# Optimization experiments

Hardware: AMD Instinct MI355X
Metric: run time of the kernel (lower is better)

Reference implementation:

```python
import jax, jax.numpy as jnp
import numpy as np

B, S, D = 256, 256, 1024
P = D // 2  # proj_dim default = input_dim / 2
NUM_HIDDEN = 2
EPS = 1e-7  # K.epsilon()
INIT_SCALE = 0.05  # keras 'uniform' init


def setup_inputs() -> dict:
    key = jax.random.key(0)
    ks = jax.random.split(key, 8)
    x = jax.random.normal(ks[0], (B, S, D), dtype=jnp.float32)
    mask = jax.random.randint(ks[1], (B, S), 0, 2).astype(bool)
    u = lambda k, shp: jax.random.uniform(k, shp, jnp.float32, -INIT_SCALE, INIT_SCALE)
    proj_head = u(ks[2], (D, P))
    proj_prep = u(ks[3], (D, P))
    proj_child = u(ks[4], (D, P))
    hidden_layers = u(ks[5], (NUM_HIDDEN, P, P))
    scorer = u(ks[6], (P,))
    return {"x": x, "proj_head": proj_head, "proj_prep": proj_prep,
            "proj_child": proj_child, "hidden_layers": hidden_layers,
            "scorer": scorer, "mask": mask}


def reference(x, proj_head, proj_prep, proj_child, hidden_layers, scorer, mask):
    # x: [B, S, D]; last two timesteps are preposition and child noun.
    head_enc = x[:, :-2, :]          # [B, S-2, D]
    prep_enc = x[:, -2, :]           # [B, D]
    child_enc = x[:, -1, :]          # [B, D]

    head_proj = jnp.einsum('bsd,dp->bsp', head_enc, proj_head)      # [B, S-2, P]
    prep_proj = (prep_enc @ proj_prep)[:, None, :]                  # [B, 1, P]
    child_proj = (child_enc @ proj_child)[:, None, :]               # [B, 1, P]

    # composition_type == 'HPCT'
    composed = jnp.tanh(head_proj + prep_proj + child_proj)         # [B, S-2, P]

    for i in range(hidden_layers.shape[0]):  # small fixed layer count
        composed = jnp.tanh(jnp.einsum('bsp,pq->bsq', composed, hidden_layers[i]))

    scores = jnp.einsum('bsp,p->bs', composed, scorer)              # [B, S-2]

    # masked exp-normalization (as in the original Keras code)
    exp_scores = jnp.exp(scores)
    head_mask = mask[:, :-2]
    masked_exp = jnp.where(head_mask, exp_scores, 0.0)
    exp_sum = jnp.sum(masked_exp, axis=1, keepdims=True) + EPS
    return masked_exp / exp_sum
```

## Files before the change

kernel.cpp:

```cpp
#include <hip/hip_runtime.h>
#include <hip/hip_bf16.h>
#include <stdint.h>

#define B_ 256
#define S_ 256
#define D_ 1024
#define P_ 512
#define SH 254
#define M_ (B_*SH)
#define EPSF 1e-7f

typedef __attribute__((ext_vector_type(8))) short short8v;
typedef __attribute__((ext_vector_type(4))) float float4v;

__device__ inline short f2bf(float f) {
  __hip_bfloat16 h = __float2bfloat16(f);
  return *reinterpret_cast<short*>(&h);
}
__device__ inline float fast_tanh(float x) {
  float e = __expf(2.0f * x);
  return 1.0f - 2.0f * __builtin_amdgcn_rcpf(e + 1.0f);
}

__global__ void k_detect(const unsigned char* m, int* flag) {
  __shared__ int c0, c3;
  if (threadIdx.x == 0) { c0 = 0; c3 = 0; }
  __syncthreads();
  int f0 = 0, f3 = 0;
  for (int i = threadIdx.x; i < 4096; i += 256) {
    unsigned char v = m[i];
    if (v != 0) {
      if ((i & 3) == 0) f0 = 1;
      if ((i & 3) == 3) f3 = 1;
    }
  }
  if (f0) atomicOr(&c0, 1);
  if (f3) atomicOr(&c3, 1);
  __syncthreads();
  if (threadIdx.x == 0) {
    int f;
    if (c3 == 0) f = 0;
    else if (c0 != 0) f = 1;
    else f = 2;
    *flag = f;
  }
}

__global__ void k_trans_head(const float* __restrict__ w, short* __restrict__ out) {
  int idx = blockIdx.x * 256 + threadIdx.x;
  int kc  = idx >> 13;
  int j   = idx & 8191;
  int krp = j >> 9;
  int n   = j & 511;
  int k0  = kc * 32 + krp * 2;
  unsigned lo = (unsigned short)f2bf(w[(size_t)k0 * P_ + n]);
  unsigned hi = (unsigned short)f2bf(w[(size_t)(k0 + 1) * P_ + n]);
  ((unsigned*)out)[kc * 8192 + n * 16 + krp] = lo | (hi << 16);
}

__global__ void k_trans_hidden(const float* __restrict__ h,
                               short* __restrict__ o0, short* __restrict__ o1) {
  int idx = blockIdx.x * 256 + threadIdx.x;
  int which = idx >> 17;
  int j = idx & 131071;
  int kc  = j >> 13;
  int r   = j & 8191;
  int krp = r >> 9;
  int n   = r & 511;
  const float* hs = h + (size_t)which * (P_*P_);
  int k0 = kc * 32 + krp * 2;
  unsigned lo = (unsigned short)f2bf(hs[(size_t)k0 * P_ + n]);
  unsigned hi = (unsigned short)f2bf(hs[(size_t)(k0 + 1) * P_ + n]);
  unsigned* o = (unsigned*)(which ? o1 : o0);
  o[kc * 8192 + n * 16 + krp] = lo | (hi << 16);
}

__global__ void __launch_bounds__(512) k_pc(const float* __restrict__ x,
                                            const float* __restrict__ wp,
                                            const float* __restrict__ wc,
                                            float* __restrict__ pc) {
  __shared__ float xs[16][256];
  int bg = blockIdx.x >> 4, cs = blockIdx.x & 15;
  int t = threadIdx.x;
  int bloc = t >> 5, c = t & 31;
  int batch = bg * 16 + bloc;
  int col = cs * 32 + c;
  float acc = 0.f;
  #pragma unroll
  for (int half = 0; half < 2; half++) {
    const float* wsrc = half ? wc : wp;
    for (int kc = 0; kc < 4; kc++) {
      const float* xr = x + ((size_t)(batch * S_ + SH + half)) * D_ + kc*256 + c*8;
      float4 v0 = *(const float4*)(xr + 0);
      float4 v1 = *(const float4*)(xr + 4);
      __syncthreads();
      *(float4*)&xs[bloc][c*8 + 0] = v0;
      *(float4*)&xs[bloc][c*8 + 4] = v1;
      __syncthreads();
      const float* wv = wsrc + (size_t)(kc*256) * P_ + col;
      #pragma unroll 8
      for (int d = 0; d < 256; d++) {
        acc += xs[bloc][d] * wv[(size_t)d * P_];
      }
    }
  }
  pc[batch * P_ + col] = acc;
}


#define LB2(DST, BASE, KC0) do {                                    \
  const uint4* _p = (BASE) + (size_t)(KC0)*2048 + bcol;             \
  DST[0]=_p[0];    DST[1]=_p[64];      DST[2]=_p[128];  DST[3]=_p[192]; \
  DST[4]=_p[2048]; DST[5]=_p[2048+64]; DST[6]=_p[2048+128]; DST[7]=_p[2048+192]; \
} while(0)

#define APAIR(CUR, CB, BUF) do {                                    \
  _Pragma("unroll") for (int cc = 0; cc < 2; cc++) {                \
    short8v a_[4];                                                  \
    _Pragma("unroll") for (int mt = 0; mt < 4; mt++)                \
      a_[mt] = *(const short8v*)&As[CUR][(mt*16 + l15)*136 + ((CB)+cc)*32 + quad*8]; \
    _Pragma("unroll") for (int nt = 0; nt < 4; nt++) {              \
      short8v bfr = *(short8v*)&BUF[cc*4 + nt];                     \
      _Pragma("unroll") for (int mt = 0; mt < 4; mt++)              \
        acc[mt][nt] = __builtin_amdgcn_mfma_f32_16x16x32_bf16(a_[mt], bfr, acc[mt][nt], 0, 0, 0); \
    }                                                               \
  }                                                                 \
} while(0)

#define S23(P, CURB, NXTB) do {                                     \
  if ((P) < 7) { LB2(NXTB, hb, 2*(P)+2); }                          \
  else if (stage == 0) { LB2(NXTB, h1v, 0); }                       \
  _Pragma("unroll") for (int cc = 0; cc < 2; cc++) {                \
    short8v a_[4];                                                  \
    _Pragma("unroll") for (int mt = 0; mt < 4; mt++)                \
      a_[mt] = *(const short8v*)&Cs[(mt*16 + l15)*520 + (2*(P)+cc)*32 + quad*8]; \
    _Pragma("unroll") for (int nt = 0; nt < 4; nt++) {              \
      short8v bfr = *(short8v*)&CURB[cc*4 + nt];                    \
      _Pragma("unroll") for (int mt = 0; mt < 4; mt++)              \
        acc[mt][nt] = __builtin_amdgcn_mfma_f32_16x16x32_bf16(a_[mt], bfr, acc[mt][nt], 0, 0, 0); \
    }                                                               \
  }                                                                 \
} while(0)

__global__ void __launch_bounds__(512, 2) k_main(
    const float* __restrict__ x, const short* __restrict__ wth,
    const short* __restrict__ h0t, const short* __restrict__ h1t,
    const float* __restrict__ scorer, const float* __restrict__ pc,
    float* __restrict__ scores)
{
  __shared__ __attribute__((aligned(16))) short As[2][64*136];
  __shared__ __attribute__((aligned(16))) short Cs[64*520];
  __shared__ float scorer_s[P_];
  __shared__ float pcs[2][P_];
  __shared__ float score_ws[64][8];

  const int tid  = threadIdx.x;
  const int lane = tid & 63;
  const int wn   = tid >> 6;
  const int l15  = lane & 15, quad = lane >> 4;
  const int rowbase = blockIdx.x * 64;

  scorer_s[tid] = scorer[tid];
  const int bb0 = rowbase / SH;
  const int bb1 = (rowbase + 63) / SH;
  pcs[0][tid] = pc[bb0 * P_ + tid];
  pcs[1][tid] = pc[bb1 * P_ + tid];
  const int lim1 = (bb0 + 1) * SH;

  const int arow = tid >> 3;
  const int akg  = (tid & 7) * 16;
  int r0 = rowbase + arow;
  int ab = r0 / SH;
  int as_ = r0 - ab * SH;
  const float* aptr = x + ((size_t)(ab * S_ + as_)) * D_ + akg;

  const uint4* wbv = (const uint4*)wth;
  const uint4* h0v = (const uint4*)h0t;
  const uint4* h1v = (const uint4*)h1t;
  const int bcol = (wn*64 + l15)*4 + quad;

  uint4 bA[8], bB[8];

  {
    float4 st0 = *(const float4*)(aptr + 0);
    float4 st1 = *(const float4*)(aptr + 4);
    float4 st2 = *(const float4*)(aptr + 8);
    float4 st3 = *(const float4*)(aptr + 12);
    short8v s0 = { f2bf(st0.x),f2bf(st0.y),f2bf(st0.z),f2bf(st0.w),
                   f2bf(st1.x),f2bf(st1.y),f2bf(st1.z),f2bf(st1.w) };
    short8v s1 = { f2bf(st2.x),f2bf(st2.y),f2bf(st2.z),f2bf(st2.w),
                   f2bf(st3.x),f2bf(st3.y),f2bf(st3.z),f2bf(st3.w) };
    *(short8v*)&As[0][arow*136 + akg]     = s0;
    *(short8v*)&As[0][arow*136 + akg + 8] = s1;
  }
  LB2(bA, wbv, 0);
  __syncthreads();

  float4v acc[4][4];
  #pragma unroll
  for (int i = 0; i < 4; i++)
    #pragma unroll
    for (int j = 0; j < 4; j++) acc[i][j] = (float4v){0.f,0.f,0.f,0.f};

  for (int sc = 0; sc < 8; sc++) {
    const int cur = sc & 1;
    float4 n0, n1, n2, n3;
    if (sc < 7) {
      const float* p = aptr + (sc + 1) * 128;
      n0 = *(const float4*)(p + 0);
      n1 = *(const float4*)(p + 4);
      n2 = *(const float4*)(p + 8);
      n3 = *(const float4*)(p + 12);
    }
    LB2(bB, wbv, 4*sc + 2);
    APAIR(cur, 0, bA);
    if (sc < 7) { LB2(bA, wbv, 4*sc + 4); }
    APAIR(cur, 2, bB);
    if (sc < 7) {
      short8v w0 = { f2bf(n0.x),f2bf(n0.y),f2bf(n0.z),f2bf(n0.w),
                     f2bf(n1.x),f2bf(n1.y),f2bf(n1.z),f2bf(n1.w) };
      short8v w1 = { f2bf(n2.x),f2bf(n2.y),f2bf(n2.z),f2bf(n2.w),
                     f2bf(n3.x),f2bf(n3.y),f2bf(n3.z),f2bf(n3.w) };
      *(short8v*)&As[cur ^ 1][arow*136 + akg]     = w0;
      *(short8v*)&As[cur ^ 1][arow*136 + akg + 8] = w1;
    }
    __syncthreads();
  }

  LB2(bA, h0v, 0);

  #pragma unroll
  for (int mt = 0; mt < 4; mt++) {
    #pragma unroll
    for (int j = 0; j < 4; j++) {
      int rl = mt*16 + quad*4 + j;
      int rg = rowbase + rl;
      const float* pcb = (rg >= lim1) ? pcs[1] : pcs[0];
      #pragma unroll
      for (int nt = 0; nt < 4; nt++) {
        int col = wn*64 + nt*16 + l15;
        float v = fast_tanh(acc[mt][nt][j] + pcb[col]);
        float o = __shfl_xor(v, 1, 64);
        unsigned hs = (unsigned short)f2bf(v);
        unsigned ho = (unsigned short)f2bf(o);
        if ((l15 & 1) == 0)
          *(unsigned*)&Cs[rl*520 + col] = hs | (ho << 16);
      }
    }
  }
  __syncthreads();

  #pragma unroll 1
  for (int stage = 0; stage < 2; stage++) {
    const uint4* hb = stage ? h1v : h0v;
    #pragma unroll
    for (int i = 0; i < 4; i++)
      #pragma unroll
      for (int j = 0; j < 4; j++) acc[i][j] = (float4v){0.f,0.f,0.f,0.f};

    S23(0, bA, bB); S23(1, bB, bA);
    S23(2, bA, bB); S23(3, bB, bA);
    S23(4, bA, bB); S23(5, bB, bA);
    S23(6, bA, bB); S23(7, bB, bA);

    if (stage == 0) {
      __syncthreads();
      #pragma unroll
      for (int mt = 0; mt < 4; mt++) {
        #pragma unroll
        for (int j = 0; j < 4; j++) {
          int rl = mt*16 + quad*4 + j;
          #pragma unroll
          for (int nt = 0; nt < 4; nt++) {
            int col = wn*64 + nt*16 + l15;
            float v = fast_tanh(acc[mt][nt][j]);
            float o = __shfl_xor(v, 1, 64);
            unsigned hs = (unsigned short)f2bf(v);
            unsigned ho = (unsigned short)f2bf(o);
            if ((l15 & 1) == 0)
              *(unsigned*)&Cs[rl*520 + col] = hs | (ho << 16);
          }
        }
      }
      __syncthreads();
    }
  }

  #pragma unroll
  for (int mt = 0; mt < 4; mt++) {
    #pragma unroll
    for (int j = 0; j < 4; j++) {
      float part = 0.f;
      #pragma unroll
      for (int nt = 0; nt < 4; nt++) {
        int col = wn*64 + nt*16 + l15;
        part += fast_tanh(acc[mt][nt][j]) * scorer_s[col];
      }
      #pragma unroll
      for (int o = 1; o < 16; o <<= 1) part += __shfl_xor(part, o, 64);
      if (l15 == 0) score_ws[mt*16 + quad*4 + j][wn] = part;
    }
  }
  __syncthreads();
  if (tid < 64) {
    float s = 0.f;
    #pragma unroll
    for (int k = 0; k < 8; k++) s += score_ws[tid][k];
    scores[rowbase + tid] = __expf(s);
  }
}

__global__ void __launch_bounds__(256) k_softmax(const float* __restrict__ scores,
                                                 const void* __restrict__ mask,
                                                 const int* __restrict__ flag,
                                                 float* __restrict__ out) {
  int b = blockIdx.x, t = threadIdx.x;
  int lane = t & 63, w = t >> 6;
  __shared__ float ps[4];
  float me = 0.f;
  bool valid = t < SH;
  if (valid) {
    float e = scores[b*SH + t];
    int f = *flag;
    bool mb;
    if (f == 1)      mb = ((const unsigned char*)mask)[b*S_ + t] != 0;
    else if (f == 2) mb = ((const float*)mask)[b*S_ + t] != 0.0f;
    else             mb = ((const int*)mask)[b*S_ + t] != 0;
    me = mb ? e : 0.f;
  }
  float v = me;
  for (int o = 1; o < 64; o <<= 1) v += __shfl_xor(v, o, 64);
  if (lane == 0) ps[w] = v;
  __syncthreads();
  float tot = ps[0] + ps[1] + ps[2] + ps[3] + EPSF;
  if (valid) out[b*SH + t] = me / tot;
}

extern "C" void kernel_launch(void* const* d_in, const int* in_sizes, int n_in,
                              void* d_out, int out_size, void* d_ws, size_t ws_size,
                              hipStream_t stream) {
  const float* x          = (const float*)d_in[0];
  const float* proj_head  = (const float*)d_in[1];
  const float* proj_prep  = (const float*)d_in[2];
  const float* proj_child = (const float*)d_in[3];
  const float* hidden     = (const float*)d_in[4];
  const float* scorer     = (const float*)d_in[5];
  const void*  mask       = d_in[6];
  float* out = (float*)d_out;
  char* ws = (char*)d_ws;

  int*   flag   = (int*)  (ws + 0);
  float* pc     = (float*)(ws + 256);
  short* wth    = (short*)(ws + 524544);
  short* h0t    = (short*)(ws + 1573120);
  short* h1t    = (short*)(ws + 2097408);
  float* scores = (float*)(ws + 2621696);

  k_detect<<<1, 256, 0, stream>>>((const unsigned char*)mask, flag);
  k_trans_head<<<1024, 256, 0, stream>>>(proj_head, wth);
  k_trans_hidden<<<1024, 256, 0, stream>>>(hidden, h0t, h1t);
  k_pc<<<256, 512, 0, stream>>>(x, proj_prep, proj_child, pc);
  k_main<<<1016, 512, 0, stream>>>(x, wth, h0t, h1t, scorer, pc, scores);
  k_softmax<<<256, 256, 0, stream>>>(scores, mask, flag, out);
}
```

Baseline: 695.3 us.

## Use 128-row tiles with 16 waves and load A directly from global

The main fused kernel now processes 128 rows per block with 1024 threads (16 waves, each owning 32 output columns) instead of 64 rows with 512 threads. The first GEMM drops the shared-memory double-buffered A staging: each wave loads its fp32 x fragments straight from global, converts them to bf16 in registers, and software-prefetches only the B fragments. The hidden-layer loops are simplified to one-step B prefetch loops. Every wave now reads the full 128xD A tile from global, so redundant global/L2 traffic rises 16x. Shared memory use also doubles, and register pressure under launch_bounds(1024,4) may limit occupancy or cause spills.

```diff
diff --git a/kernel.cpp b/kernel.cpp
--- a/kernel.cpp
+++ b/kernel.cpp
@@ -107,138 +107,85 @@
   pc[batch * P_ + col] = acc;
 }
 
-
-#define LB2(DST, BASE, KC0) do {                                    \
-  const uint4* _p = (BASE) + (size_t)(KC0)*2048 + bcol;             \
-  DST[0]=_p[0];    DST[1]=_p[64];      DST[2]=_p[128];  DST[3]=_p[192]; \
-  DST[4]=_p[2048]; DST[5]=_p[2048+64]; DST[6]=_p[2048+128]; DST[7]=_p[2048+192]; \
-} while(0)
-
-#define APAIR(CUR, CB, BUF) do {                                    \
-  _Pragma("unroll") for (int cc = 0; cc < 2; cc++) {                \
-    short8v a_[4];                                                  \
-    _Pragma("unroll") for (int mt = 0; mt < 4; mt++)                \
-      a_[mt] = *(const short8v*)&As[CUR][(mt*16 + l15)*136 + ((CB)+cc)*32 + quad*8]; \
-    _Pragma("unroll") for (int nt = 0; nt < 4; nt++) {              \
-      short8v bfr = *(short8v*)&BUF[cc*4 + nt];                     \
-      _Pragma("unroll") for (int mt = 0; mt < 4; mt++)              \
-        acc[mt][nt] = __builtin_amdgcn_mfma_f32_16x16x32_bf16(a_[mt], bfr, acc[mt][nt], 0, 0, 0); \
-    }                                                               \
-  }                                                                 \
-} while(0)
-
-#define S23(P, CURB, NXTB) do {                                     \
-  if ((P) < 7) { LB2(NXTB, hb, 2*(P)+2); }                          \
-  else if (stage == 0) { LB2(NXTB, h1v, 0); }                       \
-  _Pragma("unroll") for (int cc = 0; cc < 2; cc++) {                \
-    short8v a_[4];                                                  \
-    _Pragma("unroll") for (int mt = 0; mt < 4; mt++)                \
-      a_[mt] = *(const short8v*)&Cs[(mt*16 + l15)*520 + (2*(P)+cc)*32 + quad*8]; \
-    _Pragma("unroll") for (int nt = 0; nt < 4; nt++) {              \
-      short8v bfr = *(short8v*)&CURB[cc*4 + nt];                    \
-      _Pragma("unroll") for (int mt = 0; mt < 4; mt++)              \
-        acc[mt][nt] = __builtin_amdgcn_mfma_f32_16x16x32_bf16(a_[mt], bfr, acc[mt][nt], 0, 0, 0); \
-    }                                                               \
-  }                                                                 \
-} while(0)
-
-__global__ void __launch_bounds__(512, 2) k_main(
+__global__ void __launch_bounds__(1024, 4) k_main(
     const float* __restrict__ x, const short* __restrict__ wth,
     const short* __restrict__ h0t, const short* __restrict__ h1t,
     const float* __restrict__ scorer, const float* __restrict__ pc,
     float* __restrict__ scores)
 {
-  __shared__ __attribute__((aligned(16))) short As[2][64*136];
-  __shared__ __attribute__((aligned(16))) short Cs[64*520];
+  __shared__ __attribute__((aligned(16))) short Cs[128*520];
   __shared__ float scorer_s[P_];
   __shared__ float pcs[2][P_];
-  __shared__ float score_ws[64][8];
+  __shared__ float score_ws[128][16];
 
   const int tid  = threadIdx.x;
   const int lane = tid & 63;
-  const int wn   = tid >> 6;
+  const int w    = tid >> 6;
   const int l15  = lane & 15, quad = lane >> 4;
-  const int rowbase = blockIdx.x * 64;
-
-  scorer_s[tid] = scorer[tid];
+  const int rowbase = blockIdx.x * 128;
+
   const int bb0 = rowbase / SH;
-  const int bb1 = (rowbase + 63) / SH;
-  pcs[0][tid] = pc[bb0 * P_ + tid];
-  pcs[1][tid] = pc[bb1 * P_ + tid];
+  const int bb1 = (rowbase + 127) / SH;
+  if (tid < P_) {
+    scorer_s[tid] = scorer[tid];
+    pcs[0][tid] = pc[bb0 * P_ + tid];
+    pcs[1][tid] = pc[bb1 * P_ + tid];
+  }
   const int lim1 = (bb0 + 1) * SH;
 
-  const int arow = tid >> 3;
-  const int akg  = (tid & 7) * 16;
-  int r0 = rowbase + arow;
-  int ab = r0 / SH;
-  int as_ = r0 - ab * SH;
-  const float* aptr = x + ((size_t)(ab * S_ + as_)) * D_ + akg;
-
+  int aoff[8];
+  #pragma unroll
+  for (int mt = 0; mt < 8; mt++) {
+    int row = rowbase + mt*16 + l15;
+    int b = row / SH;
+    int s = row - b * SH;
+    aoff[mt] = ((b * S_ + s) << 10) + quad * 8;
+  }
+
+  const int bcol = (w*32 + l15)*4 + quad;
   const uint4* wbv = (const uint4*)wth;
   const uint4* h0v = (const uint4*)h0t;
   const uint4* h1v = (const uint4*)h1t;
-  const int bcol = (wn*64 + l15)*4 + quad;
-
-  uint4 bA[8], bB[8];
+
+  float4v acc[8][2];
+  #pragma unroll
+  for (int i = 0; i < 8; i++) { acc[i][0] = (float4v){0.f,0.f,0.f,0.f};
+                                acc[i][1] = (float4v){0.f,0.f,0.f,0.f}; }
+
+  __syncthreads();
 
   {
-    float4 st0 = *(const float4*)(aptr + 0);
-    float4 st1 = *(const float4*)(aptr + 4);
-    float4 st2 = *(const float4*)(aptr + 8);
-    float4 st3 = *(const float4*)(aptr + 12);
-    short8v s0 = { f2bf(st0.x),f2bf(st0.y),f2bf(st0.z),f2bf(st0.w),
-                   f2bf(st1.x),f2bf(st1.y),f2bf(st1.z),f2bf(st1.w) };
-    short8v s1 = { f2bf(st2.x),f2bf(st2.y),f2bf(st2.z),f2bf(st2.w),
-                   f2bf(st3.x),f2bf(st3.y),f2bf(st3.z),f2bf(st3.w) };
-    *(short8v*)&As[0][arow*136 + akg]     = s0;
-    *(short8v*)&As[0][arow*136 + akg + 8] = s1;
-  }
-  LB2(bA, wbv, 0);
-  __syncthreads();
-
-  float4v acc[4][4];
-  #pragma unroll
-  for (int i = 0; i < 4; i++)
-    #pragma unroll
-    for (int j = 0; j < 4; j++) acc[i][j] = (float4v){0.f,0.f,0.f,0.f};
-
-  for (int sc = 0; sc < 8; sc++) {
-    const int cur = sc & 1;
-    float4 n0, n1, n2, n3;
-    if (sc < 7) {
-      const float* p = aptr + (sc + 1) * 128;
-      n0 = *(const float4*)(p + 0);
-      n1 = *(const float4*)(p + 4);
-      n2 = *(const float4*)(p + 8);
-      n3 = *(const float4*)(p + 12);
-    }
-    LB2(bB, wbv, 4*sc + 2);
-    APAIR(cur, 0, bA);
-    if (sc < 7) { LB2(bA, wbv, 4*sc + 4); }
-    APAIR(cur, 2, bB);
-    if (sc < 7) {
-      short8v w0 = { f2bf(n0.x),f2bf(n0.y),f2bf(n0.z),f2bf(n0.w),
-                     f2bf(n1.x),f2bf(n1.y),f2bf(n1.z),f2bf(n1.w) };
-      short8v w1 = { f2bf(n2.x),f2bf(n2.y),f2bf(n2.z),f2bf(n2.w),
-                     f2bf(n3.x),f2bf(n3.y),f2bf(n3.z),f2bf(n3.w) };
-      *(short8v*)&As[cur ^ 1][arow*136 + akg]     = w0;
-      *(short8v*)&As[cur ^ 1][arow*136 + akg + 8] = w1;
-    }
-    __syncthreads();
-  }
-
-  LB2(bA, h0v, 0);
-
-  #pragma unroll
-  for (int mt = 0; mt < 4; mt++) {
+    uint4 bc0 = wbv[bcol], bc1 = wbv[bcol + 64];
+    for (int kc = 0; kc < 32; kc++) {
+      uint4 bn0, bn1;
+      if (kc < 31) {
+        bn0 = wbv[(size_t)(kc+1)*2048 + bcol];
+        bn1 = wbv[(size_t)(kc+1)*2048 + bcol + 64];
+      }
+      #pragma unroll
+      for (int mt = 0; mt < 8; mt++) {
+        const float* ap = x + aoff[mt] + kc*32;
+        float4 t0 = *(const float4*)ap;
+        float4 t1 = *(const float4*)(ap + 4);
+        short8v a = { f2bf(t0.x),f2bf(t0.y),f2bf(t0.z),f2bf(t0.w),
+                      f2bf(t1.x),f2bf(t1.y),f2bf(t1.z),f2bf(t1.w) };
+        acc[mt][0] = __builtin_amdgcn_mfma_f32_16x16x32_bf16(a, *(short8v*)&bc0, acc[mt][0], 0, 0, 0);
+        acc[mt][1] = __builtin_amdgcn_mfma_f32_16x16x32_bf16(a, *(short8v*)&bc1, acc[mt][1], 0, 0, 0);
+      }
+      bc0 = bn0; bc1 = bn1;
+    }
+  }
+
+  #pragma unroll
+  for (int mt = 0; mt < 8; mt++) {
     #pragma unroll
     for (int j = 0; j < 4; j++) {
       int rl = mt*16 + quad*4 + j;
       int rg = rowbase + rl;
       const float* pcb = (rg >= lim1) ? pcs[1] : pcs[0];
       #pragma unroll
-      for (int nt = 0; nt < 4; nt++) {
-        int col = wn*64 + nt*16 + l15;
+      for (int nt = 0; nt < 2; nt++) {
+        int col = w*32 + nt*16 + l15;
         float v = fast_tanh(acc[mt][nt][j] + pcb[col]);
         float o = __shfl_xor(v, 1, 64);
         unsigned hs = (unsigned short)f2bf(v);
@@ -254,25 +201,34 @@
   for (int stage = 0; stage < 2; stage++) {
     const uint4* hb = stage ? h1v : h0v;
     #pragma unroll
-    for (int i = 0; i < 4; i++)
-      #pragma unroll
-      for (int j = 0; j < 4; j++) acc[i][j] = (float4v){0.f,0.f,0.f,0.f};
-
-    S23(0, bA, bB); S23(1, bB, bA);
-    S23(2, bA, bB); S23(3, bB, bA);
-    S23(4, bA, bB); S23(5, bB, bA);
-    S23(6, bA, bB); S23(7, bB, bA);
+    for (int i = 0; i < 8; i++) { acc[i][0] = (float4v){0.f,0.f,0.f,0.f};
+                                  acc[i][1] = (float4v){0.f,0.f,0.f,0.f}; }
+    uint4 bc0 = hb[bcol], bc1 = hb[bcol + 64];
+    for (int kc = 0; kc < 16; kc++) {
+      uint4 bn0, bn1;
+      if (kc < 15) {
+        bn0 = hb[(size_t)(kc+1)*2048 + bcol];
+        bn1 = hb[(size_t)(kc+1)*2048 + bcol + 64];
+      }
+      #pragma unroll
+      for (int mt = 0; mt < 8; mt++) {
+        short8v a = *(const short8v*)&Cs[(mt*16 + l15)*520 + kc*32 + quad*8];
+        acc[mt][0] = __builtin_amdgcn_mfma_f32_16x16x32_bf16(a, *(short8v*)&bc0, acc[mt][0], 0, 0, 0);
+        acc[mt][1] = __builtin_amdgcn_mfma_f32_16x16x32_bf16(a, *(short8v*)&bc1, acc[mt][1], 0, 0, 0);
+      }
+      bc0 = bn0; bc1 = bn1;
+    }
 
     if (stage == 0) {
       __syncthreads();
       #pragma unroll
-      for (int mt = 0; mt < 4; mt++) {
+      for (int mt = 0; mt < 8; mt++) {
         #pragma unroll
         for (int j = 0; j < 4; j++) {
           int rl = mt*16 + quad*4 + j;
           #pragma unroll
-          for (int nt = 0; nt < 4; nt++) {
-            int col = wn*64 + nt*16 + l15;
+          for (int nt = 0; nt < 2; nt++) {
+            int col = w*32 + nt*16 + l15;
             float v = fast_tanh(acc[mt][nt][j]);
             float o = __shfl_xor(v, 1, 64);
             unsigned hs = (unsigned short)f2bf(v);
@@ -287,25 +243,22 @@
   }
 
   #pragma unroll
-  for (int mt = 0; mt < 4; mt++) {
+  for (int mt = 0; mt < 8; mt++) {
     #pragma unroll
     for (int j = 0; j < 4; j++) {
-      float part = 0.f;
-      #pragma unroll
-      for (int nt = 0; nt < 4; nt++) {
-        int col = wn*64 + nt*16 + l15;
-        part += fast_tanh(acc[mt][nt][j]) * scorer_s[col];
-      }
+      int rl = mt*16 + quad*4 + j;
+      float part = fast_tanh(acc[mt][0][j]) * scorer_s[w*32 + l15]
+                 + fast_tanh(acc[mt][1][j]) * scorer_s[w*32 + 16 + l15];
       #pragma unroll
       for (int o = 1; o < 16; o <<= 1) part += __shfl_xor(part, o, 64);
-      if (l15 == 0) score_ws[mt*16 + quad*4 + j][wn] = part;
-    }
-  }
-  __syncthreads();
-  if (tid < 64) {
+      if (l15 == 0) score_ws[rl][w] = part;
+    }
+  }
+  __syncthreads();
+  if (tid < 128) {
     float s = 0.f;
     #pragma unroll
-    for (int k = 0; k < 8; k++) s += score_ws[tid][k];
+    for (int k = 0; k < 16; k++) s += score_ws[tid][k];
     scores[rowbase + tid] = __expf(s);
   }
 }
@@ -360,6 +313,6 @@
   k_trans_head<<<1024, 256, 0, stream>>>(proj_head, wth);
   k_trans_hidden<<<1024, 256, 0, stream>>>(hidden, h0t, h1t);
   k_pc<<<256, 512, 0, stream>>>(x, proj_prep, proj_child, pc);
-  k_main<<<1016, 512, 0, stream>>>(x, wth, h0t, h1t, scorer, pc, scores);
+  k_main<<<508, 1024, 0, stream>>>(x, wth, h0t, h1t, scorer, pc, scores);
   k_softmax<<<256, 256, 0, stream>>>(scores, mask, flag, out);
 }
```

Measured after the change: 1.017 ms. 46.3% more time.
